# Performance work log

Measured on AMD Instinct MI355X. Metric: run time of the kernel, lower is better.

Reference implementation:

```python
import jax, jax.numpy as jnp
import numpy as np

N, E, C_IN, C_OUT, K = 50000, 800000, 64, 64, 3

def setup_inputs() -> dict:
    key = jax.random.key(0)
    k1, k2, k3, k4, k5, k6 = jax.random.split(key, 6)
    x = jax.random.normal(k1, (N, C_IN), dtype=jnp.float32)
    row = jax.random.randint(k2, (E,), 0, N)
    col = jax.random.randint(k3, (E,), 0, N)
    # PyG ChebConv removes self loops; avoid generating them
    col = jnp.where(col == row, (col + 1) % N, col)
    edge_index = jnp.stack([row, col])
    edge_weight = jax.random.uniform(k4, (E,), dtype=jnp.float32)
    # ChebConv learned params: one [C_in, C_out] matrix per Chebyshev order, plus bias
    W = jax.random.normal(k5, (K, C_IN, C_OUT), dtype=jnp.float32) / np.sqrt(C_IN).astype(np.float32)
    b = jax.random.normal(k6, (C_OUT,), dtype=jnp.float32) * 0.01
    return {"x": x, "edge_index": edge_index, "edge_weight": edge_weight, "W": W, "b": b}


def reference(x, edge_index, edge_weight, W, b):
    row, col = edge_index[0], edge_index[1]
    # PyG ChebConv.__norm__ with sym normalization and lambda_max = 2.0:
    # L_hat = (2/lambda_max) * (I - D^{-1/2} A D^{-1/2}) - I = -D^{-1/2} A D^{-1/2}
    deg = jax.ops.segment_sum(edge_weight, row, num_segments=N)
    dis = jnp.where(deg > 0, jax.lax.rsqrt(deg), 0.0)  # deg_inv_sqrt, inf -> 0
    w = -dis[row] * edge_weight * dis[col]             # [E] normalized Laplacian weights

    def prop(h):  # sparse matvec: L_hat @ h, [N, C]
        return jax.ops.segment_sum(w[:, None] * h[col], row, num_segments=N)

    # Chebyshev recurrence: T0 = x, T1 = L_hat x, Tk = 2 L_hat T_{k-1} - T_{k-2}
    Tx0 = x
    out = Tx0 @ W[0]
    Tx1 = prop(Tx0)
    out = out + Tx1 @ W[1]
    for k in range(2, K):
        Tx2 = 2.0 * prop(Tx1) - Tx0
        out = out + Tx2 @ W[k]
        Tx0, Tx1 = Tx1, Tx2
    return jax.nn.relu(out + b)
```

## Files before the change

kernel.cpp:

```cpp
#include <hip/hip_runtime.h>
#include <hip/hip_bf16.h>

#define C 64
#define NCOPY 8
#define FXSCALE 16777216.0f
#define LOW44 ((1ULL << 44) - 1)

typedef unsigned short u16;

__device__ __forceinline__ u16 f2bf_rne(float v) {
    unsigned u = __float_as_uint(v);
    u += 0x7FFFu + ((u >> 16) & 1u);
    return (u16)(u >> 16);
}
__device__ __forceinline__ float bf2f(u16 u) {
    return __uint_as_float((unsigned)u << 16);
}

__global__ __launch_bounds__(256) void hist8_kernel(const int* __restrict__ row,
                                                    const float* __restrict__ ew,
                                                    unsigned long long* __restrict__ cd8,
                                                    int* __restrict__ rank,
                                                    const float* __restrict__ x,
                                                    u16* __restrict__ xh,
                                                    int E, int N, int total4, int nthreads) {
    int t = threadIdx.x;
    int base = blockIdx.x * 1024;
    int copy = blockIdx.x & (NCOPY - 1);
    size_t cb = (size_t)copy * N;

    unsigned long long old[4];
    int e[4];
#pragma unroll
    for (int u = 0; u < 4; u++) {
        e[u] = base + u * 256 + t;
        if (e[u] < E) {
            int r = row[e[u]];
            unsigned long long fx = (unsigned long long)__float2uint_rn(ew[e[u]] * FXSCALE);
            unsigned long long inc = (1ULL << 44) | fx;
            old[u] = atomicAdd(&cd8[cb + r], inc);
        }
    }
#pragma unroll
    for (int u = 0; u < 4; u++) {
        if (e[u] < E) rank[e[u]] = (int)(old[u] >> 44);
    }

    int gtid = blockIdx.x * 256 + t;
    for (int i = gtid; i < total4; i += nthreads) {
        float4 v = *(const float4*)(x + (size_t)i * 4);
        ushort4 o;
        o.x = f2bf_rne(v.x); o.y = f2bf_rne(v.y);
        o.z = f2bf_rne(v.z); o.w = f2bf_rne(v.w);
        *(ushort4*)(xh + (size_t)i * 4) = o;
    }
}

__global__ __launch_bounds__(256) void scanA_kernel(const unsigned long long* __restrict__ cd8,
                                                    int* __restrict__ cnt,
                                                    float* __restrict__ dis,
                                                    int* __restrict__ bsum, int N) {
    __shared__ int s[256];
    int t = threadIdx.x;
    int i = blockIdx.x * 256 + t;
    int cv = 0;
    unsigned long long dfx = 0;
    if (i < N) {
#pragma unroll
        for (int c = 0; c < NCOPY; c++) {
            unsigned long long v = cd8[(size_t)c * N + i];
            cv += (int)(v >> 44);
            dfx += (v & LOW44);
        }
        cnt[i] = cv;
        float dv = (float)dfx * (1.0f / FXSCALE);
        dis[i] = (dv > 0.0f) ? rsqrtf(dv) : 0.0f;
    }
    s[t] = cv;
    __syncthreads();
    for (int off = 128; off > 0; off >>= 1) {
        if (t < off) s[t] += s[t + off];
        __syncthreads();
    }
    if (t == 0) bsum[blockIdx.x] = s[0];
}

__global__ __launch_bounds__(256) void scanB_kernel(int* __restrict__ bsum,
                                                    int* __restrict__ rowptr,
                                                    int G, int N) {
    __shared__ int s[256];
    int t = threadIdx.x;
    int v = (t < G) ? bsum[t] : 0;
    s[t] = v;
    __syncthreads();
    for (int off = 1; off < 256; off <<= 1) {
        int u = (t >= off) ? s[t - off] : 0;
        __syncthreads();
        s[t] += u;
        __syncthreads();
    }
    if (t < G) bsum[t] = s[t] - v;
    if (t == 255) rowptr[N] = s[255];
}

__global__ __launch_bounds__(256) void scanC_kernel(const int* __restrict__ cnt,
                                                    const unsigned long long* __restrict__ cd8,
                                                    int* __restrict__ start8,
                                                    const int* __restrict__ bsum,
                                                    int* __restrict__ rowptr, int N) {
    __shared__ int s[256];
    int t = threadIdx.x;
    int i = blockIdx.x * 256 + t;
    int v = (i < N) ? cnt[i] : 0;
    s[t] = v;
    __syncthreads();
    for (int off = 1; off < 256; off <<= 1) {
        int u = (t >= off) ? s[t - off] : 0;
        __syncthreads();
        s[t] += u;
        __syncthreads();
    }
    if (i < N) {
        int rp = bsum[blockIdx.x] + s[t] - v;
        rowptr[i] = rp;
        int run = rp;
#pragma unroll
        for (int c = 0; c < NCOPY; c++) {
            int tmp = (int)(cd8[(size_t)c * N + i] >> 44);
            start8[(size_t)c * N + i] = run;
            run += tmp;
        }
    }
}

__global__ __launch_bounds__(256) void scatter_kernel(const int* __restrict__ row,
                                                      const int* __restrict__ col,
                                                      const float* __restrict__ ew,
                                                      const float* __restrict__ dis,
                                                      const int* __restrict__ start8,
                                                      const int* __restrict__ rank,
                                                      float2* __restrict__ ewc,
                                                      int E, int N) {
    int t = threadIdx.x;
    int base = blockIdx.x * 1024;
    int copy = blockIdx.x & (NCOPY - 1);
    size_t cb = (size_t)copy * N;
#pragma unroll
    for (int u = 0; u < 4; u++) {
        int e = base + u * 256 + t;
        if (e < E) {
            int r = row[e];
            int c = col[e];
            float wv = -dis[r] * ew[e] * dis[c];
            int pos = start8[cb + r] + rank[e];
            ewc[pos] = make_float2(wv, __int_as_float(c));
        }
    }
}

__global__ __launch_bounds__(256) void spmm_csr_kernel(
        const int* __restrict__ rowptr,
        const float2* __restrict__ ewc,
        const unsigned* __restrict__ h32,
        float* __restrict__ out32,
        unsigned* __restrict__ outbf,
        int N) {
    int wid = (blockIdx.x * blockDim.x + threadIdx.x) >> 6;
    int lane = threadIdx.x & 63;
    if (wid >= N) return;
    int half = lane >> 5;
    int cp   = lane & 31;
    int beg = rowptr[wid];
    int end = rowptr[wid + 1];
    float ax0 = 0.f, ay0 = 0.f, ax1 = 0.f, ay1 = 0.f;
    float ax2 = 0.f, ay2 = 0.f, ax3 = 0.f, ay3 = 0.f;
    for (int base = beg; base < end; base += 64) {
        int idx = base + lane;
        float2 ed = (idx < end) ? ewc[idx] : make_float2(0.0f, __int_as_float(0));
        int cnt = end - base; if (cnt > 64) cnt = 64;
        for (int j = 0; j < cnt; j += 8) {
            int s0 = j + half;
            int s1 = j + 2 + half;
            int s2 = j + 4 + half;
            int s3 = j + 6 + half;
            float w0 = __shfl(ed.x, s0);
            int   c0 = __shfl(__float_as_int(ed.y), s0);
            float w1 = __shfl(ed.x, s1);
            int   c1 = __shfl(__float_as_int(ed.y), s1);
            float w2 = __shfl(ed.x, s2);
            int   c2 = __shfl(__float_as_int(ed.y), s2);
            float w3 = __shfl(ed.x, s3);
            int   c3 = __shfl(__float_as_int(ed.y), s3);
            unsigned hv0 = h32[(size_t)c0 * 32 + cp];
            unsigned hv1 = h32[(size_t)c1 * 32 + cp];
            unsigned hv2 = h32[(size_t)c2 * 32 + cp];
            unsigned hv3 = h32[(size_t)c3 * 32 + cp];
            ax0 = fmaf(w0, bf2f((u16)(hv0 & 0xffffu)), ax0);
            ay0 = fmaf(w0, bf2f((u16)(hv0 >> 16)),     ay0);
            ax1 = fmaf(w1, bf2f((u16)(hv1 & 0xffffu)), ax1);
            ay1 = fmaf(w1, bf2f((u16)(hv1 >> 16)),     ay1);
            ax2 = fmaf(w2, bf2f((u16)(hv2 & 0xffffu)), ax2);
            ay2 = fmaf(w2, bf2f((u16)(hv2 >> 16)),     ay2);
            ax3 = fmaf(w3, bf2f((u16)(hv3 & 0xffffu)), ax3);
            ay3 = fmaf(w3, bf2f((u16)(hv3 >> 16)),     ay3);
        }
    }
    float ax = (ax0 + ax1) + (ax2 + ax3);
    float ay = (ay0 + ay1) + (ay2 + ay3);
    float bx = __shfl(ax, cp + 32);
    float by = __shfl(ay, cp + 32);
    if (half == 0) {
        float rx = ax + bx;
        float ry = ay + by;
        *(float2*)(out32 + (size_t)wid * C + 2 * cp) = make_float2(rx, ry);
        unsigned pk = (unsigned)f2bf_rne(rx) | ((unsigned)f2bf_rne(ry) << 16);
        outbf[(size_t)wid * 32 + cp] = pk;
    }
}

__global__ __launch_bounds__(256) void final_gemm_kernel(
        const float* __restrict__ x,
        const float* __restrict__ T1,
        const float* __restrict__ P,
        const float* __restrict__ W,
        const float* __restrict__ b,
        float* __restrict__ out, int N) {
    __shared__ float As[16][64];
    __shared__ float Ws[16][64];

    int t  = threadIdx.x;
    int tx = t & 15;
    int ty = t >> 4;
    int n0 = blockIdx.x * 64;

    int sn = t >> 2;
    int skb = (t & 3) * 4;

    float acc[4][4];
#pragma unroll
    for (int i = 0; i < 4; i++)
#pragma unroll
        for (int j = 0; j < 4; j++) acc[i][j] = 0.0f;

#pragma unroll 1
    for (int s = 0; s < 12; s++) {
        float4 wv = *(const float4*)(W + s * 1024 + t * 4);
        int nn = n0 + sn;
        float4 av = make_float4(0.f, 0.f, 0.f, 0.f);
        if (nn < N) {
            if (s < 4) {
                av = *(const float4*)(x + (size_t)nn * C + s * 16 + skb);
            } else if (s < 8) {
                av = *(const float4*)(T1 + (size_t)nn * C + (s - 4) * 16 + skb);
            } else {
                float4 pv = *(const float4*)(P + (size_t)nn * C + (s - 8) * 16 + skb);
                float4 xv = *(const float4*)(x + (size_t)nn * C + (s - 8) * 16 + skb);
                av = make_float4(2.0f * pv.x - xv.x, 2.0f * pv.y - xv.y,
                                 2.0f * pv.z - xv.z, 2.0f * pv.w - xv.w);
            }
        }
        __syncthreads();
        {
            int wk = (t * 4) >> 6;
            int wc = (t * 4) & 63;
            *(float4*)&Ws[wk][wc] = wv;
        }
        As[skb + 0][sn] = av.x;
        As[skb + 1][sn] = av.y;
        As[skb + 2][sn] = av.z;
        As[skb + 3][sn] = av.w;
        __syncthreads();

#pragma unroll
        for (int kk = 0; kk < 16; kk++) {
            float4 a4 = *(const float4*)&As[kk][ty * 4];
            float4 w4 = *(const float4*)&Ws[kk][tx * 4];
            float ar[4] = {a4.x, a4.y, a4.z, a4.w};
            float wr[4] = {w4.x, w4.y, w4.z, w4.w};
#pragma unroll
            for (int i = 0; i < 4; i++)
#pragma unroll
                for (int j = 0; j < 4; j++)
                    acc[i][j] = fmaf(ar[i], wr[j], acc[i][j]);
        }
    }

    float4 bv = *(const float4*)(b + tx * 4);
    float br[4] = {bv.x, bv.y, bv.z, bv.w};
#pragma unroll
    for (int i = 0; i < 4; i++) {
        int node = n0 + ty * 4 + i;
        if (node < N) {
            float4 o;
            o.x = fmaxf(acc[i][0] + br[0], 0.0f);
            o.y = fmaxf(acc[i][1] + br[1], 0.0f);
            o.z = fmaxf(acc[i][2] + br[2], 0.0f);
            o.w = fmaxf(acc[i][3] + br[3], 0.0f);
            *(float4*)(out + (size_t)node * C + tx * 4) = o;
        }
    }
}

extern "C" void kernel_launch(void* const* d_in, const int* in_sizes, int n_in,
                              void* d_out, int out_size, void* d_ws, size_t ws_size,
                              hipStream_t stream) {
    const float* x  = (const float*)d_in[0];
    const int*   ei = (const int*)d_in[1];
    const float* ew = (const float*)d_in[2];
    const float* W  = (const float*)d_in[3];
    const float* b  = (const float*)d_in[4];
    float* out = (float*)d_out;

    const int N = in_sizes[0] / C;
    const int E = in_sizes[2];
    const int* row = ei;
    const int* col = ei + E;

    char* ws = (char*)d_ws;
    size_t off = 0;
    auto alloc = [&](size_t bytes) {
        void* p = ws + off;
        off = (off + bytes + 255) & ~(size_t)255;
        return p;
    };
    float*  dis    = (float*)alloc((size_t)N * 4);
    int*    cnt    = (int*)alloc((size_t)N * 4);
    int*    rowptr = (int*)alloc((size_t)(N + 1) * 4);
    float2* ewc    = (float2*)alloc((size_t)E * 8);
    float*  T1     = (float*)alloc((size_t)N * C * 4);
    float*  P      = (float*)alloc((size_t)N * C * 4);
    int*    bsum   = (int*)alloc((size_t)256 * 4);
    unsigned long long* cd8 = (unsigned long long*)alloc((size_t)NCOPY * N * 8);
    int*    start8 = (int*)alloc((size_t)NCOPY * N * 4);
    int*    rank   = (int*)alloc((size_t)E * 4);
    u16*    xh     = (u16*)alloc((size_t)N * C * 2);
    u16*    T1h    = (u16*)alloc((size_t)N * C * 2);
    u16*    Ph     = (u16*)alloc((size_t)N * C * 2);

    hipMemsetAsync(cd8, 0, (size_t)NCOPY * N * 8, stream);

    const int B = 256;
    const int G = (N + B - 1) / B;

    int histBlocks = (E + 1023) / 1024;
    int total4 = N * C / 4;
    hist8_kernel<<<histBlocks, B, 0, stream>>>(row, ew, cd8, rank, x, xh,
                                               E, N, total4, histBlocks * B);
    scanA_kernel<<<G, B, 0, stream>>>(cd8, cnt, dis, bsum, N);
    scanB_kernel<<<1, B, 0, stream>>>(bsum, rowptr, G, N);
    scanC_kernel<<<G, B, 0, stream>>>(cnt, cd8, start8, bsum, rowptr, N);
    scatter_kernel<<<histBlocks, B, 0, stream>>>(row, col, ew, dis, start8,
                                                 rank, ewc, E, N);

    int spmm_blocks = (int)(((long long)N * 64 + B - 1) / B);
    spmm_csr_kernel<<<spmm_blocks, B, 0, stream>>>(rowptr, ewc, (const unsigned*)xh,
                                                   T1, (unsigned*)T1h, N);
    spmm_csr_kernel<<<spmm_blocks, B, 0, stream>>>(rowptr, ewc, (const unsigned*)T1h,
                                                   P, (unsigned*)Ph, N);

    final_gemm_kernel<<<(N + 63) / 64, B, 0, stream>>>(x, T1, P, W, b, out, N);
}
```

Measured before the change: 204.3 us.

## Replace global-atomic CSR build with two-pass bucketed radix sort

Edge-to-CSR construction no longer uses 64-bit global atomics over 8 replicated per-row counters. It now does a two-level radix sort: per-block shared-memory histograms over buckets of 256 rows, a column-wise scan, a scatter into buckets, then a per-bucket local sort that also builds rowptr and degrees. The normalized weights are computed in a separate pass. Row and column are packed into 16 bits each, which assumes N ≤ 65536 and also masks the column in the SpMM. This removes global atomic contention and the memset, at the cost of an extra payload buffer and more passes over the edges.

```diff
diff --git a/kernel.cpp b/kernel.cpp
--- a/kernel.cpp
+++ b/kernel.cpp
@@ -2,11 +2,10 @@
 #include <hip/hip_bf16.h>
 
 #define C 64
-#define NCOPY 8
-#define FXSCALE 16777216.0f
-#define LOW44 ((1ULL << 44) - 1)
 
 typedef unsigned short u16;
+typedef unsigned int u32;
+typedef unsigned long long u64;
 
 __device__ __forceinline__ u16 f2bf_rne(float v) {
     unsigned u = __float_as_uint(v);
@@ -17,36 +16,30 @@
     return __uint_as_float((unsigned)u << 16);
 }
 
-__global__ __launch_bounds__(256) void hist8_kernel(const int* __restrict__ row,
-                                                    const float* __restrict__ ew,
-                                                    unsigned long long* __restrict__ cd8,
-                                                    int* __restrict__ rank,
-                                                    const float* __restrict__ x,
-                                                    u16* __restrict__ xh,
-                                                    int E, int N, int total4, int nthreads) {
-    int t = threadIdx.x;
-    int base = blockIdx.x * 1024;
-    int copy = blockIdx.x & (NCOPY - 1);
-    size_t cb = (size_t)copy * N;
-
-    unsigned long long old[4];
-    int e[4];
+
+__global__ __launch_bounds__(256) void p1hist_kernel(const int* __restrict__ row,
+                                                     u32* __restrict__ hoff,
+                                                     const float* __restrict__ x,
+                                                     u16* __restrict__ xh,
+                                                     int E, int NB, int total4, int nthreads) {
+    __shared__ u32 h[256];
+    int t = threadIdx.x;
+    int b = blockIdx.x;
+    h[t] = 0;
+    __syncthreads();
+    int base = b * 1024;
 #pragma unroll
     for (int u = 0; u < 4; u++) {
-        e[u] = base + u * 256 + t;
-        if (e[u] < E) {
-            int r = row[e[u]];
-            unsigned long long fx = (unsigned long long)__float2uint_rn(ew[e[u]] * FXSCALE);
-            unsigned long long inc = (1ULL << 44) | fx;
-            old[u] = atomicAdd(&cd8[cb + r], inc);
-        }
-    }
-#pragma unroll
-    for (int u = 0; u < 4; u++) {
-        if (e[u] < E) rank[e[u]] = (int)(old[u] >> 44);
-    }
-
-    int gtid = blockIdx.x * 256 + t;
+        int e = base + u * 256 + t;
+        if (e < E) {
+            int r = row[e];
+            atomicAdd(&h[r >> 8], 1u);
+        }
+    }
+    __syncthreads();
+    hoff[(size_t)b * 256 + t] = h[t];
+
+    int gtid = b * 256 + t;
     for (int i = gtid; i < total4; i += nthreads) {
         float4 v = *(const float4*)(x + (size_t)i * 4);
         ushort4 o;
@@ -56,104 +49,148 @@
     }
 }
 
-__global__ __launch_bounds__(256) void scanA_kernel(const unsigned long long* __restrict__ cd8,
-                                                    int* __restrict__ cnt,
-                                                    float* __restrict__ dis,
-                                                    int* __restrict__ bsum, int N) {
-    __shared__ int s[256];
-    int t = threadIdx.x;
-    int i = blockIdx.x * 256 + t;
-    int cv = 0;
-    unsigned long long dfx = 0;
-    if (i < N) {
-#pragma unroll
-        for (int c = 0; c < NCOPY; c++) {
-            unsigned long long v = cd8[(size_t)c * N + i];
-            cv += (int)(v >> 44);
-            dfx += (v & LOW44);
-        }
-        cnt[i] = cv;
-        float dv = (float)dfx * (1.0f / FXSCALE);
-        dis[i] = (dv > 0.0f) ? rsqrtf(dv) : 0.0f;
-    }
-    s[t] = cv;
-    __syncthreads();
-    for (int off = 128; off > 0; off >>= 1) {
-        if (t < off) s[t] += s[t + off];
-        __syncthreads();
-    }
-    if (t == 0) bsum[blockIdx.x] = s[0];
-}
-
-__global__ __launch_bounds__(256) void scanB_kernel(int* __restrict__ bsum,
-                                                    int* __restrict__ rowptr,
-                                                    int G, int N) {
-    __shared__ int s[256];
-    int t = threadIdx.x;
-    int v = (t < G) ? bsum[t] : 0;
+__global__ __launch_bounds__(256) void scanA_kernel(u32* __restrict__ hoff,
+                                                    u32* __restrict__ T, int NB) {
+    __shared__ u32 s[256];
+    int t = threadIdx.x;
+    int d = blockIdx.x;
+    u32 carry = 0;
+    int nchunk = (NB + 255) / 256;
+    for (int ch = 0; ch < nchunk; ch++) {
+        int idx = ch * 256 + t;
+        u32 v = (idx < NB) ? hoff[(size_t)idx * 256 + d] : 0;
+        s[t] = v;
+        __syncthreads();
+        for (int off = 1; off < 256; off <<= 1) {
+            u32 u = (t >= off) ? s[t - off] : 0;
+            __syncthreads();
+            s[t] += u;
+            __syncthreads();
+        }
+        if (idx < NB) hoff[(size_t)idx * 256 + d] = carry + s[t] - v;
+        u32 tot = s[255];
+        __syncthreads();
+        carry += tot;
+    }
+    if (t == 0) T[d] = carry;
+}
+
+__global__ __launch_bounds__(256) void scanB_kernel(const u32* __restrict__ T,
+                                                    u32* __restrict__ Tpre,
+                                                    int* __restrict__ rowptr, int N) {
+    __shared__ u32 s[256];
+    int t = threadIdx.x;
+    u32 v = T[t];
     s[t] = v;
     __syncthreads();
     for (int off = 1; off < 256; off <<= 1) {
-        int u = (t >= off) ? s[t - off] : 0;
+        u32 u = (t >= off) ? s[t - off] : 0;
         __syncthreads();
         s[t] += u;
         __syncthreads();
     }
-    if (t < G) bsum[t] = s[t] - v;
-    if (t == 255) rowptr[N] = s[255];
-}
-
-__global__ __launch_bounds__(256) void scanC_kernel(const int* __restrict__ cnt,
-                                                    const unsigned long long* __restrict__ cd8,
-                                                    int* __restrict__ start8,
-                                                    const int* __restrict__ bsum,
-                                                    int* __restrict__ rowptr, int N) {
-    __shared__ int s[256];
-    int t = threadIdx.x;
-    int i = blockIdx.x * 256 + t;
-    int v = (i < N) ? cnt[i] : 0;
-    s[t] = v;
-    __syncthreads();
-    for (int off = 1; off < 256; off <<= 1) {
-        int u = (t >= off) ? s[t - off] : 0;
-        __syncthreads();
-        s[t] += u;
-        __syncthreads();
-    }
-    if (i < N) {
-        int rp = bsum[blockIdx.x] + s[t] - v;
-        rowptr[i] = rp;
-        int run = rp;
-#pragma unroll
-        for (int c = 0; c < NCOPY; c++) {
-            int tmp = (int)(cd8[(size_t)c * N + i] >> 44);
-            start8[(size_t)c * N + i] = run;
-            run += tmp;
-        }
-    }
-}
-
-__global__ __launch_bounds__(256) void scatter_kernel(const int* __restrict__ row,
-                                                      const int* __restrict__ col,
-                                                      const float* __restrict__ ew,
-                                                      const float* __restrict__ dis,
-                                                      const int* __restrict__ start8,
-                                                      const int* __restrict__ rank,
-                                                      float2* __restrict__ ewc,
-                                                      int E, int N) {
-    int t = threadIdx.x;
-    int base = blockIdx.x * 1024;
-    int copy = blockIdx.x & (NCOPY - 1);
-    size_t cb = (size_t)copy * N;
+    Tpre[t] = s[t] - v;
+    if (t == 255) {
+        Tpre[256] = s[255];
+        rowptr[N] = (int)s[255];
+    }
+}
+
+__global__ __launch_bounds__(256) void p1scatter_kernel(const int* __restrict__ row,
+                                                        const int* __restrict__ col,
+                                                        const float* __restrict__ ew,
+                                                        const u32* __restrict__ hoff,
+                                                        const u32* __restrict__ Tpre,
+                                                        u64* __restrict__ pay,
+                                                        int E) {
+    __shared__ u32 cur[256];
+    int t = threadIdx.x;
+    int b = blockIdx.x;
+    cur[t] = Tpre[t] + hoff[(size_t)b * 256 + t];
+    __syncthreads();
+    int base = b * 1024;
 #pragma unroll
     for (int u = 0; u < 4; u++) {
         int e = base + u * 256 + t;
         if (e < E) {
-            int r = row[e];
-            int c = col[e];
-            float wv = -dis[r] * ew[e] * dis[c];
-            int pos = start8[cb + r] + rank[e];
-            ewc[pos] = make_float2(wv, __int_as_float(c));
+            u32 r = (u32)row[e];
+            u32 c = (u32)col[e];
+            u32 rc = (r << 16) | c;
+            u32 pos = atomicAdd(&cur[r >> 8], 1u);
+            pay[pos] = ((u64)rc << 32) | (u64)__float_as_uint(ew[e]);
+        }
+    }
+}
+
+__global__ __launch_bounds__(256) void p2_kernel(const u64* __restrict__ pay,
+                                                 const u32* __restrict__ Tpre,
+                                                 int* __restrict__ rowptr,
+                                                 float* __restrict__ dis,
+                                                 float2* __restrict__ ewc,
+                                                 int N) {
+    __shared__ u32 h[256];
+    __shared__ u32 s[256];
+    __shared__ u32 cur[256];
+    __shared__ float dsum[256];
+    int t = threadIdx.x;
+    int bk = blockIdx.x;
+    u32 base = Tpre[bk];
+    u32 cnt = Tpre[bk + 1] - base;
+
+    h[t] = 0;
+    dsum[t] = 0.0f;
+    __syncthreads();
+    for (u32 j = t; j < cnt; j += 256) {
+        u64 v = pay[base + j];
+        u32 lr = (u32)(v >> 48) & 255u;
+        atomicAdd(&h[lr], 1u);
+    }
+    __syncthreads();
+    u32 hv = h[t];
+    s[t] = hv;
+    __syncthreads();
+    for (int off = 1; off < 256; off <<= 1) {
+        u32 u = (t >= off) ? s[t - off] : 0;
+        __syncthreads();
+        s[t] += u;
+        __syncthreads();
+    }
+    u32 p = s[t] - hv;
+    int r = bk * 256 + t;
+    if (r < N) rowptr[r] = (int)(base + p);
+    cur[t] = base + p;
+    __syncthreads();
+    for (u32 j = t; j < cnt; j += 256) {
+        u64 v = pay[base + j];
+        u32 rc = (u32)(v >> 32);
+        u32 lr = (rc >> 16) & 255u;
+        float w = __uint_as_float((u32)v);
+        u32 pos = atomicAdd(&cur[lr], 1u);
+        ewc[pos] = make_float2(w, __uint_as_float(rc));
+        atomicAdd(&dsum[lr], w);
+    }
+    __syncthreads();
+    if (r < N) {
+        float dv = dsum[t];
+        dis[r] = (dv > 0.0f) ? rsqrtf(dv) : 0.0f;
+    }
+}
+
+__global__ __launch_bounds__(256) void wnorm_kernel(float2* __restrict__ ewc,
+                                                    const float* __restrict__ dis,
+                                                    int E) {
+    int t = threadIdx.x;
+    int base = blockIdx.x * 1024;
+#pragma unroll
+    for (int u = 0; u < 4; u++) {
+        int e = base + u * 256 + t;
+        if (e < E) {
+            float2 f = ewc[e];
+            u32 rc = __float_as_uint(f.y);
+            u32 r = rc >> 16;
+            u32 c = rc & 0xffffu;
+            float w = -dis[r] * f.x * dis[c];
+            ewc[e] = make_float2(w, f.y);
         }
     }
 }
@@ -184,13 +221,13 @@
             int s2 = j + 4 + half;
             int s3 = j + 6 + half;
             float w0 = __shfl(ed.x, s0);
-            int   c0 = __shfl(__float_as_int(ed.y), s0);
+            int   c0 = __shfl(__float_as_int(ed.y), s0) & 0xffff;
             float w1 = __shfl(ed.x, s1);
-            int   c1 = __shfl(__float_as_int(ed.y), s1);
+            int   c1 = __shfl(__float_as_int(ed.y), s1) & 0xffff;
             float w2 = __shfl(ed.x, s2);
-            int   c2 = __shfl(__float_as_int(ed.y), s2);
+            int   c2 = __shfl(__float_as_int(ed.y), s2) & 0xffff;
             float w3 = __shfl(ed.x, s3);
-            int   c3 = __shfl(__float_as_int(ed.y), s3);
+            int   c3 = __shfl(__float_as_int(ed.y), s3) & 0xffff;
             unsigned hv0 = h32[(size_t)c0 * 32 + cp];
             unsigned hv1 = h32[(size_t)c1 * 32 + cp];
             unsigned hv2 = h32[(size_t)c2 * 32 + cp];
@@ -323,34 +360,31 @@
         off = (off + bytes + 255) & ~(size_t)255;
         return p;
     };
+    const int NB = (E + 1023) / 1024;
+    const int NBUCK = (N + 255) / 256;
+
     float*  dis    = (float*)alloc((size_t)N * 4);
-    int*    cnt    = (int*)alloc((size_t)N * 4);
     int*    rowptr = (int*)alloc((size_t)(N + 1) * 4);
     float2* ewc    = (float2*)alloc((size_t)E * 8);
+    u64*    pay    = (u64*)alloc((size_t)E * 8);
     float*  T1     = (float*)alloc((size_t)N * C * 4);
     float*  P      = (float*)alloc((size_t)N * C * 4);
-    int*    bsum   = (int*)alloc((size_t)256 * 4);
-    unsigned long long* cd8 = (unsigned long long*)alloc((size_t)NCOPY * N * 8);
-    int*    start8 = (int*)alloc((size_t)NCOPY * N * 4);
-    int*    rank   = (int*)alloc((size_t)E * 4);
+    u32*    hoff   = (u32*)alloc((size_t)NB * 256 * 4);
+    u32*    T      = (u32*)alloc((size_t)256 * 4);
+    u32*    Tpre   = (u32*)alloc((size_t)257 * 4);
     u16*    xh     = (u16*)alloc((size_t)N * C * 2);
     u16*    T1h    = (u16*)alloc((size_t)N * C * 2);
     u16*    Ph     = (u16*)alloc((size_t)N * C * 2);
 
-    hipMemsetAsync(cd8, 0, (size_t)NCOPY * N * 8, stream);
-
     const int B = 256;
-    const int G = (N + B - 1) / B;
-
-    int histBlocks = (E + 1023) / 1024;
     int total4 = N * C / 4;
-    hist8_kernel<<<histBlocks, B, 0, stream>>>(row, ew, cd8, rank, x, xh,
-                                               E, N, total4, histBlocks * B);
-    scanA_kernel<<<G, B, 0, stream>>>(cd8, cnt, dis, bsum, N);
-    scanB_kernel<<<1, B, 0, stream>>>(bsum, rowptr, G, N);
-    scanC_kernel<<<G, B, 0, stream>>>(cnt, cd8, start8, bsum, rowptr, N);
-    scatter_kernel<<<histBlocks, B, 0, stream>>>(row, col, ew, dis, start8,
-                                                 rank, ewc, E, N);
+
+    p1hist_kernel<<<NB, B, 0, stream>>>(row, hoff, x, xh, E, NB, total4, NB * B);
+    scanA_kernel<<<256, B, 0, stream>>>(hoff, T, NB);
+    scanB_kernel<<<1, B, 0, stream>>>(T, Tpre, rowptr, N);
+    p1scatter_kernel<<<NB, B, 0, stream>>>(row, col, ew, hoff, Tpre, pay, E);
+    p2_kernel<<<NBUCK, B, 0, stream>>>(pay, Tpre, rowptr, dis, ewc, N);
+    wnorm_kernel<<<NB, B, 0, stream>>>(ewc, dis, E);
 
     int spmm_blocks = (int)(((long long)N * 64 + B - 1) / B);
     spmm_csr_kernel<<<spmm_blocks, B, 0, stream>>>(rowptr, ewc, (const unsigned*)xh,
```

New measurement: 182.6 us. -10.6%, faster.
